# Optimization experiments

Hardware: AMD Instinct MI355X
Metric: run time of the kernel (lower is better)

## Reference

```python
import jax, jax.numpy as jnp
import numpy as np

B, T, NE, H = 4, 1024, 1024, 16
HS = NE // H  # 64
EPS = 0.00064


def setup_inputs() -> dict:
    key = jax.random.key(0)
    ks = jax.random.split(key, 30)
    def rn(k, shape, s):
        return jax.random.normal(k, shape, jnp.float32) * s
    d = {}
    d["x"] = jax.random.normal(ks[0], (B, T, NE), jnp.float32)
    d["time_maa_x"] = jax.random.uniform(ks[1], (NE,), jnp.float32)
    d["time_maa"] = jax.random.uniform(ks[2], (4, 1, 1, NE), jnp.float32)
    d["maa_w1"] = rn(ks[3], (128, NE), 0.02)   # 4 * D_MIX_LORA=32
    d["maa_w2"] = rn(ks[4], (4, 32, NE), 0.02)
    d["decay_w1"] = rn(ks[5], (64, NE), 0.02)
    d["decay_w2"] = rn(ks[6], (64, NE), 0.02)
    d["aaa_w1"] = rn(ks[7], (16, NE), 0.02)
    d["aaa_w2"] = rn(ks[8], (16, NE), 0.02)
    d["kkk_w1"] = rn(ks[9], (16, NE), 0.02)
    d["kkk_w2"] = rn(ks[10], (16, NE), 0.02)
    d["gate_w1"] = rn(ks[11], (128, NE), 0.02)
    d["gate_w2"] = rn(ks[12], (128, NE), 0.02)
    d["ma_w1"] = rn(ks[13], (16, NE), 0.02)
    d["ma_w2"] = rn(ks[14], (16, NE), 0.02)
    d["mk_w1"] = rn(ks[15], (16, NE), 0.02)
    d["mk_w2"] = rn(ks[16], (16, NE), 0.02)
    d["time_decay"] = jnp.linspace(-6.5, -1.5, NE, dtype=jnp.float32)  # decay_speed + 0.5 shape
    d["time_faaaa"] = rn(ks[17], (NE,), 0.02)
    d["time_aaaaa"] = rn(ks[18], (NE,), 0.02)
    d["time_misc_a"] = rn(ks[19], (NE,), 0.02)
    d["time_misc_k"] = rn(ks[20], (NE,), 0.02)
    d["Wr"] = rn(ks[21], (NE, NE), 0.5 / NE ** 0.5)
    d["Wk"] = rn(ks[22], (NE, NE), 0.05 / NE ** 0.5)
    d["Wv"] = rn(ks[23], (NE, NE), 0.5 / NE ** 0.5)
    d["Wo"] = rn(ks[24], (NE, NE), 1.0 / NE ** 0.5)
    d["ln_w"] = jnp.ones((NE,), jnp.float32)
    d["ln_b"] = jnp.zeros((NE,), jnp.float32)
    return d


def _forward(x, time_maa_x, time_maa, maa_w1, maa_w2, decay_w1, decay_w2,
             aaa_w1, aaa_w2, kkk_w1, kkk_w2, gate_w1, gate_w2,
             ma_w1, ma_w2, mk_w1, mk_w2, time_decay, time_faaaa, time_aaaaa,
             time_misc_a, time_misc_k, Wr, Wk, Wv, Wo, ln_w, ln_b):
    Bx, Tx, C = x.shape
    # token-shift delta: xx[t] = x[t-1] - x[t], with x[-1] = 0
    xx = jnp.pad(x, ((0, 0), (1, 0), (0, 0)))[:, :Tx] - x
    mix = x + xx * time_maa_x
    lo = jnp.tanh(jnp.einsum('btc,dc->btd', mix, maa_w1)).reshape(Bx, Tx, 4, 32)
    lo = jnp.einsum('btgk,gkc->gbtc', lo, maa_w2)           # [4,B,T,C]
    xm = x[None] + xx[None] * (lo + time_maa)               # time_maa broadcasts [4,1,1,C]
    xrg, xwa, xk, xv = xm[0], xm[1], xm[2], xm[3]

    r = xrg @ Wr.T
    g = jnp.tanh(xrg @ gate_w1.T) @ gate_w2
    k = xk @ Wk.T
    v = xv @ Wv.T
    w2 = jnp.tanh(xwa @ decay_w1.T) @ decay_w2
    w = -jax.nn.softplus(-(time_decay + w2)) - 0.5
    kk = k + jnp.tanh(xk @ kkk_w1.T) @ kkk_w2
    kkh = kk.reshape(Bx, Tx, H, HS)
    kk = (kkh / jnp.maximum(jnp.linalg.norm(kkh, axis=-1, keepdims=True), 1e-12)).reshape(Bx, Tx, C)
    a = jax.nn.sigmoid(time_aaaaa + (xwa @ aaa_w1.T) @ aaa_w2)
    ma = jax.nn.sigmoid(time_misc_a + (xwa @ ma_w1.T) @ ma_w2)
    k = k * ma + k * a * (1.0 - ma)
    mk = jax.nn.sigmoid(time_misc_k + (xk @ mk_w1.T) @ mk_w2)
    k = k * jnp.exp(w * mk)
    b = -kk * a

    # RWKV7 delta-rule recurrence: per-(B,H) HSxHS matrix state, scan over T
    def to_th(t):
        return t.reshape(Bx, Tx, H, HS).transpose(1, 0, 2, 3)  # [T,B,H,HS]
    qt, wt, kt, vt, at, bt = map(to_th, (r, w, k, v, kk, b))
    wt = jnp.exp(-jnp.exp(wt))

    def step(s, inp):
        q_, w_, k_, v_, a_, b_ = inp
        sa = jnp.einsum('bhij,bhj->bhi', s, a_)
        s = s * w_[:, :, None, :] + sa[..., None] * b_[:, :, None, :] + v_[..., None] * k_[:, :, None, :]
        return s, jnp.einsum('bhij,bhj->bhi', s, q_)

    s0 = jnp.zeros((Bx, H, HS, HS), x.dtype)
    _, y = jax.lax.scan(step, s0, (qt, wt, kt, vt, at, bt))
    y = y.transpose(1, 0, 2, 3).reshape(Bx, Tx, C)

    # GroupNorm with H groups, eps=0.00064
    yg = y.reshape(Bx, Tx, H, HS)
    mu = yg.mean(-1, keepdims=True)
    var = ((yg - mu) ** 2).mean(-1, keepdims=True)
    y = ((yg - mu) / jnp.sqrt(var + EPS)).reshape(Bx, Tx, C) * ln_w + ln_b

    # per-head bonus: (r.k * faaaa) v
    rk = (r.reshape(Bx, Tx, H, HS) * k.reshape(Bx, Tx, H, HS) * time_faaaa.reshape(H, HS)).sum(-1, keepdims=True)
    y = y + (rk * v.reshape(Bx, Tx, H, HS)).reshape(Bx, Tx, C)
    return (y * g) @ Wo.T


def reference(x, time_maa_x, time_maa, maa_w1, maa_w2, decay_w1, decay_w2,
              aaa_w1, aaa_w2, kkk_w1, kkk_w2, gate_w1, gate_w2,
              ma_w1, ma_w2, mk_w1, mk_w2, time_decay, time_faaaa, time_aaaaa,
              time_misc_a, time_misc_k, Wr, Wk, Wv, Wo, ln_w, ln_b):
    return _forward(x, time_maa_x, time_maa, maa_w1, maa_w2, decay_w1, decay_w2,
                    aaa_w1, aaa_w2, kkk_w1, kkk_w2, gate_w1, gate_w2,
                    ma_w1, ma_w2, mk_w1, mk_w2, time_decay, time_faaaa, time_aaaaa,
                    time_misc_a, time_misc_k, Wr, Wk, Wv, Wo, ln_w, ln_b)
```

## Files before the change

### kernel.cpp

```cpp
#include <hip/hip_runtime.h>
#include <cstdint>
#include <cstddef>

#define BB   4
#define TT   1024
#define CC   1024
#define HH   16
#define HSS  64
#define NNtok 4096
#define EPSGN 0.00064f
#define W2TS 192

typedef unsigned short bf16u;
typedef __attribute__((ext_vector_type(8))) short short8;
typedef __attribute__((ext_vector_type(4))) float f32x4;
#define SLOT 4194304ull

__device__ __forceinline__ float bf2f(bf16u u){
  union { unsigned int i; float f; } cv; cv.i = ((unsigned int)u) << 16; return cv.f;
}
__device__ __forceinline__ unsigned short f2bfbits(unsigned int x){
  return (unsigned short)((x + 0x7fffu + ((x >> 16) & 1u)) >> 16);
}
__device__ __forceinline__ bf16u f2bf(float f){
  union { float f; unsigned int i; } cv; cv.f = f;
  return f2bfbits(cv.i);
}
__device__ __forceinline__ void ld4bf(const bf16u* p, float* o){
  ushort4 u = *reinterpret_cast<const ushort4*>(p);
  o[0]=bf2f(u.x); o[1]=bf2f(u.y); o[2]=bf2f(u.z); o[3]=bf2f(u.w);
}
__device__ __forceinline__ void st4bf(bf16u* p, const float* v){
  ushort4 u; u.x=f2bf(v[0]); u.y=f2bf(v[1]); u.z=f2bf(v[2]); u.w=f2bf(v[3]);
  *reinterpret_cast<ushort4*>(p) = u;
}
__device__ __forceinline__ unsigned short f2h(float f){
  union { _Float16 h; unsigned short s; } c; c.h = (_Float16)f; return c.s;
}
__device__ __forceinline__ void st4h(bf16u* p, const float* v){
  ushort4 u; u.x=f2h(v[0]); u.y=f2h(v[1]); u.z=f2h(v[2]); u.w=f2h(v[3]);
  *reinterpret_cast<ushort4*>(p) = u;
}
__device__ __forceinline__ void ld4f(const float* p, float* o){
  float4 v = *reinterpret_cast<const float4*>(p);
  o[0]=v.x; o[1]=v.y; o[2]=v.z; o[3]=v.w;
}
__device__ __forceinline__ float sigm(float x){ return 1.f / (1.f + expf(-x)); }

__device__ __forceinline__ float bflo(unsigned int u){
  union { unsigned int i; float f; } c; c.i = u << 16; return c.f;
}
__device__ __forceinline__ float bfhi(unsigned int u){
  union { unsigned int i; float f; } c; c.i = u & 0xffff0000u; return c.f;
}
__device__ __forceinline__ float hlo(unsigned int u){
  union { unsigned short s; _Float16 h; } c; c.s = (unsigned short)(u & 0xffffu); return (float)c.h;
}
__device__ __forceinline__ float hhi(unsigned int u){
  union { unsigned short s; _Float16 h; } c; c.s = (unsigned short)(u >> 16); return (float)c.h;
}
__device__ __forceinline__ float hval(unsigned short s){
  union { unsigned short s; _Float16 h; } c; c.s = s; return (float)c.h;
}
__device__ __forceinline__ float dot4(const float* x, const float* y){
  return (x[0]*y[0] + x[1]*y[1]) + (x[2]*y[2] + x[3]*y[3]);
}

template<int CTRL>
__device__ __forceinline__ float dpp_add(float v){
  union { float f; int i; } a, b;
  a.f = v;
  b.i = __builtin_amdgcn_update_dpp(0, a.i, CTRL, 0xF, 0xF, true);
  return v + b.f;
}
__device__ __forceinline__ float red16(float v){
  v = dpp_add<0xB1>(v);
  v = dpp_add<0x4E>(v);
  v = dpp_add<0x124>(v);
  v = dpp_add<0x128>(v);
  return v;
}
__device__ __forceinline__ float red32(float v){
  v = red16(v);
  union { float f; int i; } x, y;
  x.f = v; y.f = v;
  asm volatile("" : "+v"(y.i));
  asm volatile("v_permlane16_swap_b32 %0, %1" : "+v"(x.i), "+v"(y.i));
  return x.f + y.f;
}

__global__ __launch_bounds__(256) void k_prep(const float* __restrict__ x,
                                              const float* __restrict__ tmx,
                                              bf16u* __restrict__ MIX){
  int e = (blockIdx.x * 256 + threadIdx.x) * 4;
  int n = e >> 10;
  int c = e & (CC - 1);
  int t = n & (TT - 1);
  float xf[4]; ld4f(x + e, xf);
  float pf[4] = {0.f, 0.f, 0.f, 0.f};
  if (t > 0) ld4f(x + e - CC, pf);
  float tm[4]; ld4f(tmx + c, tm);
  float mv[4];
  #pragma unroll
  for (int i = 0; i < 4; ++i) mv[i] = xf[i] + (pf[i] - xf[i]) * tm[i];
  st4bf(MIX + e, mv);
}

__global__ __launch_bounds__(256) void k_wconv1(
    const float* __restrict__ Wr, const float* __restrict__ Wk,
    const float* __restrict__ Wv,
    const float* __restrict__ maa_w1, const float* __restrict__ gate_w1,
    const float* __restrict__ decay_w1, const float* __restrict__ aaa_w1,
    const float* __restrict__ ma_w1, const float* __restrict__ kkk_w1,
    const float* __restrict__ mk_w1,
    const float* __restrict__ maa_w2, const float* __restrict__ decay_w2,
    bf16u* __restrict__ WrB, bf16u* __restrict__ WkB, bf16u* __restrict__ WvB,
    bf16u* __restrict__ W1B, bf16u* __restrict__ W2TB){
  int blk = blockIdx.x, tid = threadIdx.x;
  if (blk < 3072){
    const float* src = (blk < 1024) ? Wr : (blk < 2048) ? Wk : Wv;
    bf16u* dst = (blk < 1024) ? WrB : (blk < 2048) ? WkB : WvB;
    size_t e = (size_t)(blk & 1023) * 1024 + (size_t)tid * 4;
    float v[4]; ld4f(src + e, v);
    st4bf(dst + e, v);
  } else if (blk < 3456){
    int row = blk - 3072;
    const float* src;
    if      (row < 128) src = maa_w1   + (size_t)row * 1024;
    else if (row < 256) src = gate_w1  + (size_t)(row - 128) * 1024;
    else if (row < 320) src = decay_w1 + (size_t)(row - 256) * 1024;
    else if (row < 336) src = aaa_w1   + (size_t)(row - 320) * 1024;
    else if (row < 352) src = ma_w1    + (size_t)(row - 336) * 1024;
    else if (row < 368) src = kkk_w1   + (size_t)(row - 352) * 1024;
    else                src = mk_w1    + (size_t)(row - 368) * 1024;
    float v[4]; ld4f(src + tid * 4, v);
    st4bf(W1B + (size_t)row * 1024 + tid * 4, v);
  } else {
    int j = blk - 3456;
    const float* src = (j < 128) ? (maa_w2 + (size_t)j * 1024)
                                 : (decay_w2 + (size_t)(j - 128) * 1024);
    for (int c = tid; c < 1024; c += 256)
      W2TB[(size_t)c * W2TS + j] = f2bf(src[c]);
  }
}

__global__ __launch_bounds__(256) void k_wconv2(const float* __restrict__ Wo,
                                                const float* __restrict__ gate_w2,
                                                bf16u* __restrict__ WoB,
                                                bf16u* __restrict__ GW2T){
  int blk = blockIdx.x, tid = threadIdx.x;
  if (blk < 1024){
    size_t e = ((size_t)blk * 256 + tid) * 4;
    float v[4]; ld4f(Wo + e, v);
    st4bf(WoB + e, v);
  } else {
    int c = (blk - 1024) * 2 + (tid >> 7);
    int j = tid & 127;
    GW2T[(size_t)c * 128 + j] = f2bf(gate_w2[(size_t)j * CC + c]);
  }
}

template<bool OB>
__global__ __launch_bounds__(256) void k_gemm_mfma_b(const bf16u* __restrict__ X,
                                                     const bf16u* __restrict__ WB,
                                                     void* __restrict__ OUTv,
                                                     int Nd, int Kd, int act_n){
  __shared__ short As[2][128 * 40];
  __shared__ short Bs[2][128 * 40];
  const int tid  = threadIdx.x;
  const int lane = tid & 63;
  const int wv   = tid >> 6;
  const int wm   = wv >> 1, wn = wv & 1;
  const int bn0  = blockIdx.x * 128;
  const int bm0  = blockIdx.y * 128;
  const int l15  = lane & 15;
  const int quad = lane >> 4;

  f32x4 acc[4][4];
  #pragma unroll
  for (int mi = 0; mi < 4; ++mi)
    #pragma unroll
    for (int ni = 0; ni < 4; ++ni)
      #pragma unroll
      for (int rg = 0; rg < 4; ++rg) acc[mi][ni][rg] = 0.f;

  const int r    = tid >> 1;
  const int half = (tid & 1) * 16;

  const bf16u* wsrc = (bn0 + r < Nd) ? WB + (size_t)(bn0 + r) * Kd : nullptr;
  const bf16u* xsrc = X + (size_t)(bm0 + r) * Kd;

  uint4 xa = *(const uint4*)(xsrc + half);
  uint4 xb = *(const uint4*)(xsrc + half + 8);
  uint4 wa = make_uint4(0,0,0,0), wb = wa;
  if (wsrc){
    wa = *(const uint4*)(wsrc + half);
    wb = *(const uint4*)(wsrc + half + 8);
  }
  *(uint4*)&As[0][r * 40 + half]     = xa;
  *(uint4*)&As[0][r * 40 + half + 8] = xb;
  *(uint4*)&Bs[0][r * 40 + half]     = wa;
  *(uint4*)&Bs[0][r * 40 + half + 8] = wb;
  __syncthreads();

  const int NK = Kd >> 5;
  for (int k = 0; k < NK; ++k){
    const int cur = k & 1;
    if (k + 1 < NK){
      int k0 = (k + 1) << 5;
      xa = *(const uint4*)(xsrc + k0 + half);
      xb = *(const uint4*)(xsrc + k0 + half + 8);
      if (wsrc){
        wa = *(const uint4*)(wsrc + k0 + half);
        wb = *(const uint4*)(wsrc + k0 + half + 8);
      }
    }
    short8 af[4], bfg[4];
    #pragma unroll
    for (int mi = 0; mi < 4; ++mi)
      af[mi] = *(const short8*)&As[cur][(wm*64 + mi*16 + l15) * 40 + quad*8];
    #pragma unroll
    for (int ni = 0; ni < 4; ++ni)
      bfg[ni] = *(const short8*)&Bs[cur][(wn*64 + ni*16 + l15) * 40 + quad*8];
    #pragma unroll
    for (int mi = 0; mi < 4; ++mi)
      #pragma unroll
      for (int ni = 0; ni < 4; ++ni)
        acc[mi][ni] = __builtin_amdgcn_mfma_f32_16x16x32_bf16(af[mi], bfg[ni], acc[mi][ni], 0, 0, 0);
    if (k + 1 < NK){
      const int nxt = cur ^ 1;
      *(uint4*)&As[nxt][r * 40 + half]     = xa;
      *(uint4*)&As[nxt][r * 40 + half + 8] = xb;
      *(uint4*)&Bs[nxt][r * 40 + half]     = wa;
      *(uint4*)&Bs[nxt][r * 40 + half + 8] = wb;
      __syncthreads();
    }
  }

  #pragma unroll
  for (int mi = 0; mi < 4; ++mi){
    #pragma unroll
    for (int ni = 0; ni < 4; ++ni){
      int col = bn0 + wn*64 + ni*16 + l15;
      if (col >= Nd) continue;
      #pragma unroll
      for (int rg = 0; rg < 4; ++rg){
        int row = bm0 + wm*64 + mi*16 + quad*4 + rg;
        float v = acc[mi][ni][rg];
        if (col < act_n) v = tanhf(v);
        if (OB) ((bf16u*)OUTv)[(size_t)row * Nd + col] = f2bf(v);
        else    ((float*)OUTv)[(size_t)row * Nd + col] = v;
      }
    }
  }
}

template<int KD, int EP>
__global__ __launch_bounds__(256) void k_gemm_nn_b(const bf16u* __restrict__ A, int lda,
                                                   const bf16u* __restrict__ BT, int koff,
                                                   bf16u* __restrict__ OUT,
                                                   const float* __restrict__ x,
                                                   const float* __restrict__ tma_g){
  __shared__ short As[128 * (KD + 8)];
  __shared__ short Bs[128 * (KD + 8)];
  const int tid  = threadIdx.x;
  const int lane = tid & 63;
  const int wv   = tid >> 6;
  const int wm   = wv >> 1, wn = wv & 1;
  const int bn0  = blockIdx.x * 128;
  const int bm0  = blockIdx.y * 128;
  const int l15  = lane & 15;
  const int quad = lane >> 4;

  for (int idx = tid; idx < 128 * (KD / 8); idx += 256){
    int r  = idx / (KD / 8);
    int kc = (idx % (KD / 8)) * 8;
    *(uint4*)&As[r * (KD + 8) + kc] =
        *(const uint4*)(A + (size_t)(bm0 + r) * lda + kc);
  }
  for (int idx = tid; idx < 128 * (KD / 8); idx += 256){
    int cc_ = idx / (KD / 8);
    int kc  = (idx % (KD / 8)) * 8;
    *(uint4*)&Bs[cc_ * (KD + 8) + kc] =
        *(const uint4*)(BT + (size_t)(bn0 + cc_) * W2TS + koff + kc);
  }
  __syncthreads();

  f32x4 acc[4][4];
  #pragma unroll
  for (int mi = 0; mi < 4; ++mi)
    #pragma unroll
    for (int ni = 0; ni < 4; ++ni)
      #pragma unroll
      for (int rg = 0; rg < 4; ++rg) acc[mi][ni][rg] = 0.f;

  #pragma unroll
  for (int kk = 0; kk < KD; kk += 32){
    short8 af[4], bfg[4];
    #pragma unroll
    for (int mi = 0; mi < 4; ++mi)
      af[mi] = *(const short8*)&As[(wm*64 + mi*16 + l15) * (KD + 8) + kk + quad*8];
    #pragma unroll
    for (int ni = 0; ni < 4; ++ni)
      bfg[ni] = *(const short8*)&Bs[(wn*64 + ni*16 + l15) * (KD + 8) + kk + quad*8];
    #pragma unroll
    for (int mi = 0; mi < 4; ++mi)
      #pragma unroll
      for (int ni = 0; ni < 4; ++ni)
        acc[mi][ni] = __builtin_amdgcn_mfma_f32_16x16x32_bf16(af[mi], bfg[ni], acc[mi][ni], 0, 0, 0);
  }

  #pragma unroll
  for (int mi = 0; mi < 4; ++mi){
    #pragma unroll
    for (int ni = 0; ni < 4; ++ni){
      int col = bn0 + wn*64 + ni*16 + l15;
      float tm = (EP == 1) ? tma_g[col] : 0.f;
      #pragma unroll
      for (int rg = 0; rg < 4; ++rg){
        int row = bm0 + wm*64 + mi*16 + quad*4 + rg;
        float v = acc[mi][ni][rg];
        if (EP == 1){
          float xv = x[(size_t)row * CC + col];
          float xp = ((row & (TT - 1)) == 0) ? 0.f : x[(size_t)row * CC + col - CC];
          v = xv + (xp - xv) * (v + tm);
        }
        OUT[(size_t)row * CC + col] = f2bf(v);
      }
    }
  }
}

template<bool OB>
__global__ __launch_bounds__(256) void k_gemm_mfma(const bf16u* __restrict__ X,
                                                   const float* __restrict__ Wa,
                                                   const float* __restrict__ Wb,
                                                   const float* __restrict__ Wc,
                                                   int na, int nab,
                                                   void* __restrict__ OUTv,
                                                   int Nd, int Kd, int act_n){
  __shared__ short As[128 * 40];
  __shared__ short Bs[128 * 40];
  const int tid  = threadIdx.x;
  const int lane = tid & 63;
  const int wv   = tid >> 6;
  const int wm   = wv >> 1, wn = wv & 1;
  const int bn0  = blockIdx.x * 128;
  const int bm0  = blockIdx.y * 128;
  const int l15  = lane & 15;
  const int quad = lane >> 4;

  f32x4 acc[4][4];
  #pragma unroll
  for (int mi = 0; mi < 4; ++mi)
    #pragma unroll
    for (int ni = 0; ni < 4; ++ni)
      #pragma unroll
      for (int rg = 0; rg < 4; ++rg) acc[mi][ni][rg] = 0.f;

  const int r    = tid >> 1;
  const int half = (tid & 1) * 16;

  int rr = bn0 + r;
  const float* wsrc = nullptr;
  if (rr < na)        wsrc = Wa + (size_t)rr * Kd;
  else if (rr < nab)  wsrc = Wb + (size_t)(rr - na) * Kd;
  else if (rr < Nd)   wsrc = Wc + (size_t)(rr - nab) * Kd;
  const bf16u* xsrc = X + (size_t)(bm0 + r) * Kd;

  for (int k0 = 0; k0 < Kd; k0 += 32){
    uint4 xa = *(const uint4*)(xsrc + k0 + half);
    uint4 xb = *(const uint4*)(xsrc + k0 + half + 8);
    uint4 w0 = make_uint4(0,0,0,0), w1 = w0, w2 = w0, w3 = w0;
    if (wsrc){
      w0 = *(const uint4*)(wsrc + k0 + half);
      w1 = *(const uint4*)(wsrc + k0 + half + 4);
      w2 = *(const uint4*)(wsrc + k0 + half + 8);
      w3 = *(const uint4*)(wsrc + k0 + half + 12);
    }
    union { unsigned short s[8]; uint4 v; } p0, p1;
    p0.s[0]=f2bfbits(w0.x); p0.s[1]=f2bfbits(w0.y); p0.s[2]=f2bfbits(w0.z); p0.s[3]=f2bfbits(w0.w);
    p0.s[4]=f2bfbits(w1.x); p0.s[5]=f2bfbits(w1.y); p0.s[6]=f2bfbits(w1.z); p0.s[7]=f2bfbits(w1.w);
    p1.s[0]=f2bfbits(w2.x); p1.s[1]=f2bfbits(w2.y); p1.s[2]=f2bfbits(w2.z); p1.s[3]=f2bfbits(w2.w);
    p1.s[4]=f2bfbits(w3.x); p1.s[5]=f2bfbits(w3.y); p1.s[6]=f2bfbits(w3.z); p1.s[7]=f2bfbits(w3.w);

    *(uint4*)&As[r * 40 + half]     = xa;
    *(uint4*)&As[r * 40 + half + 8] = xb;
    *(uint4*)&Bs[r * 40 + half]     = p0.v;
    *(uint4*)&Bs[r * 40 + half + 8] = p1.v;
    __syncthreads();

    short8 af[4], bfg[4];
    #pragma unroll
    for (int mi = 0; mi < 4; ++mi)
      af[mi] = *(const short8*)&As[(wm*64 + mi*16 + l15) * 40 + quad*8];
    #pragma unroll
    for (int ni = 0; ni < 4; ++ni)
      bfg[ni] = *(const short8*)&Bs[(wn*64 + ni*16 + l15) * 40 + quad*8];
    #pragma unroll
    for (int mi = 0; mi < 4; ++mi)
      #pragma unroll
      for (int ni = 0; ni < 4; ++ni)
        acc[mi][ni] = __builtin_amdgcn_mfma_f32_16x16x32_bf16(af[mi], bfg[ni], acc[mi][ni], 0, 0, 0);
    __syncthreads();
  }

  #pragma unroll
  for (int mi = 0; mi < 4; ++mi){
    #pragma unroll
    for (int ni = 0; ni < 4; ++ni){
      int col = bn0 + wn*64 + ni*16 + l15;
      if (col >= Nd) continue;
      #pragma unroll
      for (int rg = 0; rg < 4; ++rg){
        int row = bm0 + wm*64 + mi*16 + quad*4 + rg;
        float v = acc[mi][ni][rg];
        if (col < act_n) v = tanhf(v);
        if (OB) ((bf16u*)OUTv)[(size_t)row * Nd + col] = f2bf(v);
        else    ((float*)OUTv)[(size_t)row * Nd + col] = v;
      }
    }
  }
}

template<int KD, int EP>
__global__ __launch_bounds__(256) void k_gemm_nn(const bf16u* __restrict__ A, int lda,
                                                 const float* __restrict__ B,
                                                 bf16u* __restrict__ OUT,
                                                 const float* __restrict__ x,
                                                 const float* __restrict__ tma_g){
  __shared__ short As[128 * (KD + 8)];
  __shared__ short Bs[128 * (KD + 8)];
  const int tid  = threadIdx.x;
  const int lane = tid & 63;
  const int wv   = tid >> 6;
  const int wm   = wv >> 1, wn = wv & 1;
  const int bn0  = blockIdx.x * 128;
  const int bm0  = blockIdx.y * 128;
  const int l15  = lane & 15;
  const int quad = lane >> 4;

  for (int idx = tid; idx < 128 * (KD / 8); idx += 256){
    int r  = idx / (KD / 8);
    int kc = (idx % (KD / 8)) * 8;
    *(uint4*)&As[r * (KD + 8) + kc] =
        *(const uint4*)(A + (size_t)(bm0 + r) * lda + kc);
  }
  for (int idx = tid; idx < KD * 128; idx += 256){
    int k = idx >> 7, c = idx & 127;
    Bs[c * (KD + 8) + k] = (short)f2bf(B[(size_t)k * CC + bn0 + c]);
  }
  __syncthreads();

  f32x4 acc[4][4];
  #pragma unroll
  for (int mi = 0; mi < 4; ++mi)
    #pragma unroll
    for (int ni = 0; ni < 4; ++ni)
      #pragma unroll
      for (int rg = 0; rg < 4; ++rg) acc[mi][ni][rg] = 0.f;

  #pragma unroll
  for (int kk = 0; kk < KD; kk += 32){
    short8 af[4], bfg[4];
    #pragma unroll
    for (int mi = 0; mi < 4; ++mi)
      af[mi] = *(const short8*)&As[(wm*64 + mi*16 + l15) * (KD + 8) + kk + quad*8];
    #pragma unroll
    for (int ni = 0; ni < 4; ++ni)
      bfg[ni] = *(const short8*)&Bs[(wn*64 + ni*16 + l15) * (KD + 8) + kk + quad*8];
    #pragma unroll
    for (int mi = 0; mi < 4; ++mi)
      #pragma unroll
      for (int ni = 0; ni < 4; ++ni)
        acc[mi][ni] = __builtin_amdgcn_mfma_f32_16x16x32_bf16(af[mi], bfg[ni], acc[mi][ni], 0, 0, 0);
  }

  #pragma unroll
  for (int mi = 0; mi < 4; ++mi){
    #pragma unroll
    for (int ni = 0; ni < 4; ++ni){
      int col = bn0 + wn*64 + ni*16 + l15;
      float tm = (EP == 1) ? tma_g[col] : 0.f;
      #pragma unroll
      for (int rg = 0; rg < 4; ++rg){
        int row = bm0 + wm*64 + mi*16 + quad*4 + rg;
        float v = acc[mi][ni][rg];
        if (EP == 1){
          float xv = x[(size_t)row * CC + col];
          float xp = ((row & (TT - 1)) == 0) ? 0.f : x[(size_t)row * CC + col - CC];
          v = xv + (xp - xv) * (v + tm);
        }
        OUT[(size_t)row * CC + col] = f2bf(v);
      }
    }
  }
}

template<int WMODE>
__global__ __launch_bounds__(256) void k_elem(bf16u* __restrict__ K0,
    const bf16u* __restrict__ P1, const bf16u* __restrict__ P2,
    const bf16u* __restrict__ W2A,
    const float* __restrict__ kw2, const float* __restrict__ aw2,
    const float* __restrict__ maw2, const float* __restrict__ mkw2,
    const float* __restrict__ td,  const float* __restrict__ taa,
    const float* __restrict__ tma, const float* __restrict__ tmk,
    const float* __restrict__ faaaa,
    bf16u* __restrict__ KKN, bf16u* __restrict__ Bb, bf16u* __restrict__ UX,
    float* __restrict__ WF,
    bf16u* __restrict__ Rq, float* __restrict__ Dsc, float* __restrict__ RKsc){
  int n0 = blockIdx.x * 4, tid = threadIdx.x;
  __shared__ float at_l[4][16], mat_l[4][16], kt_l[4][16], mkt_l[4][16];
  {
    int grp = tid >> 6, q = tid & 63, tt = q >> 4, j = q & 15;
    if (grp == 0)      at_l[tt][j]  = bf2f(P1[(size_t)(n0+tt)*96 + 64 + j]);
    else if (grp == 1) mat_l[tt][j] = bf2f(P1[(size_t)(n0+tt)*96 + 80 + j]);
    else if (grp == 2) kt_l[tt][j]  = bf2f(P2[(size_t)(n0+tt)*32 + j]);
    else               mkt_l[tt][j] = bf2f(P2[(size_t)(n0+tt)*32 + 16 + j]);
  }
  __syncthreads();
  int c  = tid * 4;
  int h  = tid >> 4;
  int lg = tid & 15;

  float kkk[4][4], aa[4][4], mam[4][4], mkm[4][4];
  #pragma unroll
  for (int tt = 0; tt < 4; ++tt)
    #pragma unroll
    for (int i = 0; i < 4; ++i){ kkk[tt][i]=0; aa[tt][i]=0; mam[tt][i]=0; mkm[tt][i]=0; }

  #pragma unroll 4
  for (int j = 0; j < 16; ++j){
    float wk[4], wa[4], wm[4], wq[4];
    ld4f(kw2  + (size_t)j*CC + c, wk);
    ld4f(aw2  + (size_t)j*CC + c, wa);
    ld4f(maw2 + (size_t)j*CC + c, wm);
    ld4f(mkw2 + (size_t)j*CC + c, wq);
    #pragma unroll
    for (int tt = 0; tt < 4; ++tt){
      float s1 = kt_l[tt][j], s2 = at_l[tt][j], s3 = mat_l[tt][j], s4 = mkt_l[tt][j];
      #pragma unroll
      for (int i = 0; i < 4; ++i){
        kkk[tt][i] += s1 * wk[i];
        aa[tt][i]  += s2 * wa[i];
        mam[tt][i] += s3 * wm[i];
        mkm[tt][i] += s4 * wq[i];
      }
    }
  }

  float td4[4], taa4[4], tma4[4], tmk4[4], fa4[4];
  ld4f(td + c, td4); ld4f(taa + c, taa4); ld4f(tma + c, tma4); ld4f(tmk + c, tmk4);
  ld4f(faaaa + c, fa4);

#define ELEM_TOKEN(TT_, E_, A_, B_, KF_, WD_) do{ \
    float k0a[4]; ld4bf(K0 + (E_), k0a); \
    float w2a[4]; ld4bf(W2A + (E_), w2a); \
    float ssq = 0.f; \
    _Pragma("unroll") \
    for (int i = 0; i < 4; ++i){ A_[i] = k0a[i] + kkk[TT_][i]; ssq += A_[i]*A_[i]; } \
    ssq = red16(ssq); \
    float rinv = 1.f / fmaxf(sqrtf(ssq), 1e-12f); \
    float outw_[4]; \
    _Pragma("unroll") \
    for (int i = 0; i < 4; ++i){ \
      float z  = td4[i] + w2a[i]; \
      float nz = -z; \
      float sp = (nz > 15.f) ? nz : log1pf(expf(nz)); \
      float w  = -sp - 0.5f; \
      float av  = sigm(taa4[i] + aa[TT_][i]); \
      float mav = sigm(tma4[i] + mam[TT_][i]); \
      float mkv = sigm(tmk4[i] + mkm[TT_][i]); \
      A_[i] *= rinv; \
      B_[i]  = -A_[i] * av; \
      KF_[i] = k0a[i] * (mav + av * (1.f - mav)) * expf(w * mkv); \
      float ou = -expf(w); \
      outw_[i] = ou; \
      if (WMODE == 1) WD_[i] = __expf(ou);               \
      else            WD_[i] = __expf(hval(f2h(ou)));    \
    } \
    st4bf(Bb + (E_), B_); \
    st4bf(K0 + (E_), KF_); \
    if (WMODE == 1) *(float4*)(WF + (E_)) = make_float4(WD_[0], WD_[1], WD_[2], WD_[3]); \
    else            st4h(UX + (E_), outw_); \
  }while(0)

  #pragma unroll
  for (int p = 0; p < 2; ++p){
    const int ttE = 2*p, ttO = ttE + 1;
    size_t eE = (size_t)(n0 + ttE) * CC + c;
    size_t eO = eE + CC;
    float aE[4], bE[4], kfE[4], wdE[4];
    float aO[4], bO[4], kfO[4], wdO[4];
    ELEM_TOKEN(ttE, eE, aE, bE, kfE, wdE);
    ELEM_TOKEN(ttO, eO, aO, bO, kfO, wdO);
    st4bf(KKN + eE, aE);

    float rE[4], rO[4];
    ld4bf(Rq + eE, rE); ld4bf(Rq + eO, rO);

    float rkE = red16(rE[0]*kfE[0]*fa4[0] + rE[1]*kfE[1]*fa4[1]
                    + rE[2]*kfE[2]*fa4[2] + rE[3]*kfE[3]*fa4[3]);
    float rkO = red16(rO[0]*kfO[0]*fa4[0] + rO[1]*kfO[1]*fa4[1]
                    + rO[2]*kfO[2]*fa4[2] + rO[3]*kfO[3]*fa4[3]);

    float c1 = red16(dot4(bE, aO));
    float d  = red16(dot4(kfE, aO));
    float u1[4];
    #pragma unroll
    for (int i = 0; i < 4; ++i) u1[i] = wdE[i]*aO[i] + c1*aE[i];
    st4bf(KKN + eO, u1);

    float cq = red16(dot4(bE, rE));
    float e1 = red16(dot4(kfE, rE));
    float qe[4];
    #pragma unroll
    for (int i = 0; i < 4; ++i) qe[i] = wdE[i]*rE[i] + cq*aE[i];
    st4bf(Rq + eE, qe);

    float cz  = red16(dot4(bO, rO));
    float e21 = red16(dot4(kfO, rO));
    float z[4];
    #pragma unroll
    for (int i = 0; i < 4; ++i) z[i] = wdO[i]*rO[i] + cz*aO[i];
    float cy  = red16(dot4(bE, z));
    float e20 = red16(dot4(kfE, z));
    float qo[4];
    #pragma unroll
    for (int i = 0; i < 4; ++i) qo[i] = wdE[i]*z[i] + cy*aE[i];
    st4bf(Rq + eO, qo);

    if (lg == 0){
      size_t pr = (size_t)((n0 + ttE) >> 1);
      float4 dv; dv.x = d; dv.y = e1; dv.z = e20; dv.w = e21;
      *(float4*)(Dsc + (pr * HH + h) * 4) = dv;
      RKsc[(size_t)(n0 + ttE) * HH + h] = rkE;
      RKsc[(size_t)(n0 + ttO) * HH + h] = rkO;
    }
  }
#undef ELEM_TOKEN
}

template<int WMODE>
__global__ __launch_bounds__(256) void k_rec(const bf16u* __restrict__ Qp,
                                             const bf16u* __restrict__ WT,
                                             const float* __restrict__ WF,
                                             const bf16u* __restrict__ KFt,
                                             const bf16u* __restrict__ Vt,
                                             const bf16u* __restrict__ Aa,
                                             const bf16u* __restrict__ Bv,
                                             const float* __restrict__ Dsc,
                                             bf16u* __restrict__ Y){
  const int p   = blockIdx.x;
  const int g   = (p & 7) | ((p >> 6) << 3);
  const int oct = (p >> 3) & 7;
  const int b   = g >> 4;
  const int h   = g & 15;
  const int tid = threadIdx.x;
  const int l31 = tid & 31;
  const int i   = oct * 8 + (tid >> 5);
  const size_t base0 = (size_t)(b * TT) * CC + h * HSS;
  const size_t colb  = base0 + l31 * 2;
  const size_t rowb  = base0 + i;
  const size_t dscb  = ((size_t)(b * (TT/2)) * HH + h) * 4;

  float S0 = 0.f, S1 = 0.f;

  unsigned int qEA,qOA,aEA,uOA,kEA,kOA,bEA,bOA,wEA,wOA; float2 fEA,fOA; unsigned short vEA,vOA; float4 dA;
  unsigned int qEB,qOB,aEB,uOB,kEB,kOB,bEB,bOB,wEB,wOB; float2 fEB,fOB; unsigned short vEB,vOB; float4 dB;
  unsigned int qEC,qOC,aEC,uOC,kEC,kOC,bEC,bOC,wEC,wOC; float2 fEC,fOC; unsigned short vEC,vOC; float4 dC;
  unsigned int qED,qOD,aED,uOD,kED,kOD,bED,bOD,wED,wOD; float2 fED,fOD; unsigned short vED,vOD; float4 dD;

#define PL(S, T_) do{ \
    size_t cE_ = colb + (size_t)(T_) * CC, cO_ = cE_ + CC; \
    qE##S = *(const unsigned int*)(Qp  + cE_); qO##S = *(const unsigned int*)(Qp  + cO_); \
    aE##S = *(const unsigned int*)(Aa  + cE_); uO##S = *(const unsigned int*)(Aa  + cO_); \
    kE##S = *(const unsigned int*)(KFt + cE_); kO##S = *(const unsigned int*)(KFt + cO_); \
    bE##S = *(const unsigned int*)(Bv  + cE_); bO##S = *(const unsigned int*)(Bv  + cO_); \
    if (WMODE == 1){ \
      fE##S = *(const float2*)(WF + cE_); fO##S = *(const float2*)(WF + cO_); \
    } else { \
      wE##S = *(const unsigned int*)(WT + cE_); wO##S = *(const unsigned int*)(WT + cO_); \
    } \
    vE##S = Vt[rowb + (size_t)(T_) * CC]; \
    vO##S = Vt[rowb + (size_t)(T_ + 1) * CC]; \
    d##S  = *(const float4*)(Dsc + dscb + (size_t)((T_) >> 1) * (HH*4)); \
  }while(0)

#define PSTEP(S, T_) do{ \
    float a0=bflo(aE##S), a1=bfhi(aE##S); \
    float u0=bflo(uO##S), u1=bfhi(uO##S); \
    float g0=bflo(qE##S), g1=bfhi(qE##S); \
    float o0=bflo(qO##S), o1=bfhi(qO##S); \
    float pE_ = fmaf(S1, a1, S0 * a0); \
    float pO_ = fmaf(S1, u1, S0 * u0); \
    float yE_ = fmaf(S1, g1, S0 * g0); \
    float yO_ = fmaf(S1, o1, S0 * o0); \
    pE_ = red32(pE_); \
    pO_ = red32(pO_); \
    yE_ = red32(yE_); \
    yO_ = red32(yO_); \
    float vEf = bf2f(vE##S), vOf = bf2f(vO##S); \
    float saE = pE_; \
    float saO = fmaf(d##S.x, vEf, pO_); \
    float ypE = fmaf(d##S.y, vEf, yE_); \
    float ypO = fmaf(d##S.z, vEf, fmaf(d##S.w, vOf, yO_)); \
    float k0=bflo(kE##S), k1=bfhi(kE##S); \
    float b0=bflo(bE##S), b1=bfhi(bE##S); \
    float w0, w1; \
    if (WMODE == 1){ w0=fE##S.x; w1=fE##S.y; } \
    else { w0=__expf(hlo(wE##S)); w1=__expf(hhi(wE##S)); } \
    S0 = fmaf(S0, w0, fmaf(saE, b0, vEf * k0)); \
    S1 = fmaf(S1, w1, fmaf(saE, b1, vEf * k1)); \
    float ko0=bflo(kO##S), ko1=bfhi(kO##S); \
    float bo0=bflo(bO##S), bo1=bfhi(bO##S); \
    float wo0, wo1; \
    if (WMODE == 1){ wo0=fO##S.x; wo1=fO##S.y; } \
    else { wo0=__expf(hlo(wO##S)); wo1=__expf(hhi(wO##S)); } \
    S0 = fmaf(S0, wo0, fmaf(saO, bo0, vOf * ko0)); \
    S1 = fmaf(S1, wo1, fmaf(saO, bo1, vOf * ko1)); \
    if (l31 == 0){ \
      Y[rowb + (size_t)(T_) * CC]     = f2bf(ypE); \
      Y[rowb + (size_t)(T_ + 1) * CC] = f2bf(ypO); \
    } \
  }while(0)

  PL(A, 0); PL(B, 2); PL(C, 4); PL(D, 6);
  for (int t = 0; t < TT; t += 8){
    PSTEP(A, t);
    if (t + 8  < TT) PL(A, t + 8);
    PSTEP(B, t + 2);
    if (t + 10 < TT) PL(B, t + 10);
    PSTEP(C, t + 4);
    if (t + 12 < TT) PL(C, t + 12);
    PSTEP(D, t + 6);
    if (t + 14 < TT) PL(D, t + 14);
  }
#undef PL
#undef PSTEP
}

__global__ __launch_bounds__(256) void k_post(const bf16u* __restrict__ Y,
                                              const bf16u* __restrict__ Vt,
                                              const bf16u* __restrict__ GV,
                                              const float* __restrict__ lnw,
                                              const float* __restrict__ lnb,
                                              const float* __restrict__ RKsc,
                                              bf16u* __restrict__ YG){
  int n = blockIdx.x, tid = threadIdx.x;
  int c = tid * 4;
  size_t e = (size_t)n * CC + c;

  float ya[4]; ld4bf(Y + e, ya);
  float s = ya[0] + ya[1] + ya[2] + ya[3];
  s = red16(s);
  float mu = s * (1.f / 64.f);
  float d[4], vs = 0.f;
  #pragma unroll
  for (int i = 0; i < 4; ++i){ d[i] = ya[i] - mu; vs += d[i] * d[i]; }
  vs = red16(vs);
  float rstd = rsqrtf(vs * (1.f / 64.f) + EPSGN);

  float rk = RKsc[(size_t)n * HH + (tid >> 4)];

  float va[4]; ld4bf(Vt + e, va);
  float lw4[4], lb4[4];
  ld4f(lnw + c, lw4); ld4f(lnb + c, lb4);
  float g[4]; ld4bf(GV + e, g);
  float o[4];
  #pragma unroll
  for (int i = 0; i < 4; ++i){
    float yn = d[i] * rstd * lw4[i] + lb4[i] + rk * va[i];
    o[i] = yn * g[i];
  }
  st4bf(YG + e, o);
}

extern "C" void kernel_launch(void* const* d_in, const int* in_sizes, int n_in,
                              void* d_out, int out_size, void* d_ws, size_t ws_size,
                              hipStream_t stream){
  (void)in_sizes; (void)n_in; (void)out_size;
  const float* x        = (const float*)d_in[0];
  const float* tmx      = (const float*)d_in[1];
  const float* tmaa     = (const float*)d_in[2];
  const float* maa_w1   = (const float*)d_in[3];
  const float* maa_w2   = (const float*)d_in[4];
  const float* decay_w1 = (const float*)d_in[5];
  const float* decay_w2 = (const float*)d_in[6];
  const float* aaa_w1   = (const float*)d_in[7];
  const float* aaa_w2   = (const float*)d_in[8];
  const float* kkk_w1   = (const float*)d_in[9];
  const float* kkk_w2   = (const float*)d_in[10];
  const float* gate_w1  = (const float*)d_in[11];
  const float* gate_w2  = (const float*)d_in[12];
  const float* ma_w1    = (const float*)d_in[13];
  const float* ma_w2    = (const float*)d_in[14];
  const float* mk_w1    = (const float*)d_in[15];
  const float* mk_w2    = (const float*)d_in[16];
  const float* t_decay  = (const float*)d_in[17];
  const float* t_faaaa  = (const float*)d_in[18];
  const float* t_aaaaa  = (const float*)d_in[19];
  const float* t_misc_a = (const float*)d_in[20];
  const float* t_misc_k = (const float*)d_in[21];
  const float* Wr       = (const float*)d_in[22];
  const float* Wk       = (const float*)d_in[23];
  const float* Wv       = (const float*)d_in[24];
  const float* Wo       = (const float*)d_in[25];
  const float* ln_w     = (const float*)d_in[26];
  const float* ln_b     = (const float*)d_in[27];

  bf16u* bw  = (bf16u*)d_ws;
  bf16u* MIX = bw + 0*SLOT;
  bf16u* X0  = bw + 0*SLOT;
  bf16u* KKN = bw + 0*SLOT;
  bf16u* YG  = bw + 0*SLOT;
  bf16u* X1  = bw + 1*SLOT;
  bf16u* Bb  = bw + 1*SLOT;
  bf16u* GV  = bw + 1*SLOT;
  bf16u* X2  = bw + 2*SLOT;
  bf16u* UX  = bw + 2*SLOT;
  bf16u* X3  = bw + 3*SLOT;
  bf16u* W2A = bw + 3*SLOT;
  bf16u* Yb  = bw + 3*SLOT;
  bf16u* R   = bw + 4*SLOT;
  bf16u* K0  = bw + 5*SLOT;
  bf16u* V   = bw + 6*SLOT;
  char*  wsb = (char*)d_ws;
  bf16u* LO  = (bf16u*)(wsb + (56ull<<20));
  bf16u* GT  = (bf16u*)(wsb + (57ull<<20));
  bf16u* P1  = (bf16u*)(wsb + (58ull<<20));
  bf16u* P2  = (bf16u*)(wsb + (58ull<<20) + (768ull<<10));
  float* Dsc = (float*)(wsb + (59ull<<20));
  float* RKsc= (float*)(wsb + (59ull<<20) + (512ull<<10));
  float* WF  = (float*)(wsb + (60ull<<20));
  bf16u* WrB = (bf16u*)(wsb + (60ull<<20));
  bf16u* WkB = (bf16u*)(wsb + (62ull<<20));
  bf16u* WvB = (bf16u*)(wsb + (64ull<<20));
  bf16u* W1B = (bf16u*)(wsb + (66ull<<20));
  bf16u* W2TB= (bf16u*)(wsb + (67ull<<20));
  bf16u* WoB = (bf16u*)(wsb + (60ull<<20));
  bf16u* GW2T= (bf16u*)(wsb + (62ull<<20));
  const bool fast = ws_size >= (77ull<<20);

  if (fast){
    k_wconv1<<<3648, 256, 0, stream>>>(Wr, Wk, Wv, maa_w1, gate_w1, decay_w1,
                                       aaa_w1, ma_w1, kkk_w1, mk_w1,
                                       maa_w2, decay_w2,
                                       WrB, WkB, WvB, W1B, W2TB);
    k_prep<<<4096, 256, 0, stream>>>(x, tmx, MIX);
    k_gemm_mfma_b<true><<<dim3(1,32),256,0,stream>>>(MIX, W1B, LO, 128, CC, 128);
    bf16u* XMs[4] = {X0, X1, X2, X3};
    for (int g = 0; g < 4; ++g)
      k_gemm_nn_b<32,1><<<dim3(8,32),256,0,stream>>>(LO + g*32, 128, W2TB, g*32,
                                                     XMs[g], x, tmaa + (size_t)g*CC);
    k_gemm_mfma_b<true><<<dim3(8,32),256,0,stream>>>(X0, WrB, R,  CC, CC, 0);
    k_gemm_mfma_b<true><<<dim3(8,32),256,0,stream>>>(X2, WkB, K0, CC, CC, 0);
    k_gemm_mfma_b<true><<<dim3(8,32),256,0,stream>>>(X3, WvB, V,  CC, CC, 0);
    k_gemm_mfma_b<true><<<dim3(1,32),256,0,stream>>>(X0, W1B + 128*1024, GT, 128, CC, 128);
    k_gemm_mfma_b<true><<<dim3(1,32),256,0,stream>>>(X1, W1B + 256*1024, P1, 96,  CC, 64);
    k_gemm_mfma_b<true><<<dim3(1,32),256,0,stream>>>(X2, W1B + 352*1024, P2, 32,  CC, 16);
    k_gemm_nn_b<64,0><<<dim3(8,32),256,0,stream>>>(P1, 96, W2TB, 128, W2A, nullptr, nullptr);
    k_elem<1><<<1024, 256, 0, stream>>>(K0, P1, P2, W2A,
                                        kkk_w2, aaa_w2, ma_w2, mk_w2,
                                        t_decay, t_aaaaa, t_misc_a, t_misc_k, t_faaaa,
                                        KKN, Bb, UX, WF, R, Dsc, RKsc);
    k_rec<1><<<512, 256, 0, stream>>>(R, UX, WF, K0, V, KKN, Bb, Dsc, Yb);
    k_wconv2<<<1536, 256, 0, stream>>>(Wo, gate_w2, WoB, GW2T);
    k_gemm_mfma_b<true><<<dim3(8,32),256,0,stream>>>(GT, GW2T, GV, CC, 128, 0);
    k_post<<<4096, 256, 0, stream>>>(Yb, V, GV, ln_w, ln_b, RKsc, YG);
    k_gemm_mfma_b<false><<<dim3(8,32),256,0,stream>>>(YG, WoB, d_out, CC, CC, 0);
  } else {
    k_prep<<<4096, 256, 0, stream>>>(x, tmx, MIX);
    k_gemm_mfma<true><<<dim3(1,32),256,0,stream>>>(MIX, maa_w1, maa_w1, maa_w1,
                                                   128, 128, LO, 128, CC, 128);
    bf16u* XMs[4] = {X0, X1, X2, X3};
    for (int g = 0; g < 4; ++g)
      k_gemm_nn<32,1><<<dim3(8,32),256,0,stream>>>(LO + g*32, 128,
                                                   maa_w2 + (size_t)g*32*CC,
                                                   XMs[g], x, tmaa + (size_t)g*CC);
    k_gemm_mfma<true><<<dim3(8,32),256,0,stream>>>(X0, Wr, Wr, Wr, CC, CC, R,  CC, CC, 0);
    k_gemm_mfma<true><<<dim3(8,32),256,0,stream>>>(X2, Wk, Wk, Wk, CC, CC, K0, CC, CC, 0);
    k_gemm_mfma<true><<<dim3(8,32),256,0,stream>>>(X3, Wv, Wv, Wv, CC, CC, V,  CC, CC, 0);
    k_gemm_mfma<true><<<dim3(1,32),256,0,stream>>>(X0, gate_w1, gate_w1, gate_w1,
                                                   128, 128, GT, 128, CC, 128);
    k_gemm_mfma<true><<<dim3(1,32),256,0,stream>>>(X1, decay_w1, aaa_w1, ma_w1,
                                                   64, 80, P1, 96, CC, 64);
    k_gemm_mfma<true><<<dim3(1,32),256,0,stream>>>(X2, kkk_w1, mk_w1, mk_w1,
                                                   16, 32, P2, 32, CC, 16);
    k_gemm_nn<64,0><<<dim3(8,32),256,0,stream>>>(P1, 96, decay_w2, W2A, nullptr, nullptr);
    k_elem<0><<<1024, 256, 0, stream>>>(K0, P1, P2, W2A,
                                        kkk_w2, aaa_w2, ma_w2, mk_w2,
                                        t_decay, t_aaaaa, t_misc_a, t_misc_k, t_faaaa,
                                        KKN, Bb, UX, WF, R, Dsc, RKsc);
    k_rec<0><<<512, 256, 0, stream>>>(R, UX, WF, K0, V, KKN, Bb, Dsc, Yb);
    k_gemm_nn<128,0><<<dim3(8,32),256,0,stream>>>(GT, 128, gate_w2, GV, nullptr, nullptr);
    k_post<<<4096, 256, 0, stream>>>(Yb, V, GV, ln_w, ln_b, RKsc, YG);
    k_gemm_mfma<false><<<dim3(8,32),256,0,stream>>>(YG, Wo, Wo, Wo, CC, CC, d_out, CC, CC, 0);
  }
}
```

Before: 677.2 us.

## Halve GEMM M-tile to 64 rows and batch small GEMM launches via grid z

Replaces the 128x128 bf16 MFMA GEMM tile with a 64x128 tile, doubling the number of blocks for every projection GEMM so the 256 CUs get more work. The four maa mixing GEMMs are merged into one launch over blockIdx.z, and the three LoRA down-projections likewise. This targets under-occupancy and launch overhead on small grids, at the cost of less operand reuse per block (more reloads of the weight tile). The X0..X3 buffers are assumed to sit SLOT apart.

```diff
diff --git a/kernel.cpp b/kernel.cpp
--- a/kernel.cpp
+++ b/kernel.cpp
@@ -160,47 +160,45 @@
   }
 }
 
+#define B64_ASZ (64*40)
+#define B64_BSZ (128*40)
 template<bool OB>
-__global__ __launch_bounds__(256) void k_gemm_mfma_b(const bf16u* __restrict__ X,
-                                                     const bf16u* __restrict__ WB,
-                                                     void* __restrict__ OUTv,
-                                                     int Nd, int Kd, int act_n){
-  __shared__ short As[2][128 * 40];
-  __shared__ short Bs[2][128 * 40];
+__device__ __forceinline__ void gemm_b64_body(const bf16u* __restrict__ X,
+                                              const bf16u* __restrict__ WB,
+                                              void* __restrict__ OUTv,
+                                              int Nd, int Kd, int act_n,
+                                              short* __restrict__ As,
+                                              short* __restrict__ Bs,
+                                              int bn0, int bm0){
   const int tid  = threadIdx.x;
   const int lane = tid & 63;
   const int wv   = tid >> 6;
   const int wm   = wv >> 1, wn = wv & 1;
-  const int bn0  = blockIdx.x * 128;
-  const int bm0  = blockIdx.y * 128;
   const int l15  = lane & 15;
   const int quad = lane >> 4;
 
-  f32x4 acc[4][4];
-  #pragma unroll
-  for (int mi = 0; mi < 4; ++mi)
+  f32x4 acc[2][4];
+  #pragma unroll
+  for (int mi = 0; mi < 2; ++mi)
     #pragma unroll
     for (int ni = 0; ni < 4; ++ni)
       #pragma unroll
       for (int rg = 0; rg < 4; ++rg) acc[mi][ni][rg] = 0.f;
 
-  const int r    = tid >> 1;
-  const int half = (tid & 1) * 16;
-
-  const bf16u* wsrc = (bn0 + r < Nd) ? WB + (size_t)(bn0 + r) * Kd : nullptr;
-  const bf16u* xsrc = X + (size_t)(bm0 + r) * Kd;
-
-  uint4 xa = *(const uint4*)(xsrc + half);
-  uint4 xb = *(const uint4*)(xsrc + half + 8);
+  const int ra = tid >> 2, ka = (tid & 3) * 8;
+  const int rb = tid >> 1, kb = (tid & 1) * 16;
+  const bf16u* xsrc = X + (size_t)(bm0 + ra) * Kd;
+  const bf16u* wsrc = (bn0 + rb < Nd) ? WB + (size_t)(bn0 + rb) * Kd : nullptr;
+
+  uint4 xa = *(const uint4*)(xsrc + ka);
   uint4 wa = make_uint4(0,0,0,0), wb = wa;
   if (wsrc){
-    wa = *(const uint4*)(wsrc + half);
-    wb = *(const uint4*)(wsrc + half + 8);
-  }
-  *(uint4*)&As[0][r * 40 + half]     = xa;
-  *(uint4*)&As[0][r * 40 + half + 8] = xb;
-  *(uint4*)&Bs[0][r * 40 + half]     = wa;
-  *(uint4*)&Bs[0][r * 40 + half + 8] = wb;
+    wa = *(const uint4*)(wsrc + kb);
+    wb = *(const uint4*)(wsrc + kb + 8);
+  }
+  *(uint4*)&As[ra * 40 + ka]      = xa;
+  *(uint4*)&Bs[rb * 40 + kb]      = wa;
+  *(uint4*)&Bs[rb * 40 + kb + 8]  = wb;
   __syncthreads();
 
   const int NK = Kd >> 5;
@@ -208,44 +206,42 @@
     const int cur = k & 1;
     if (k + 1 < NK){
       int k0 = (k + 1) << 5;
-      xa = *(const uint4*)(xsrc + k0 + half);
-      xb = *(const uint4*)(xsrc + k0 + half + 8);
+      xa = *(const uint4*)(xsrc + k0 + ka);
       if (wsrc){
-        wa = *(const uint4*)(wsrc + k0 + half);
-        wb = *(const uint4*)(wsrc + k0 + half + 8);
+        wa = *(const uint4*)(wsrc + k0 + kb);
+        wb = *(const uint4*)(wsrc + k0 + kb + 8);
       }
     }
-    short8 af[4], bfg[4];
-    #pragma unroll
-    for (int mi = 0; mi < 4; ++mi)
-      af[mi] = *(const short8*)&As[cur][(wm*64 + mi*16 + l15) * 40 + quad*8];
+    short8 af[2], bfg[4];
+    #pragma unroll
+    for (int mi = 0; mi < 2; ++mi)
+      af[mi] = *(const short8*)&As[cur*B64_ASZ + (wm*32 + mi*16 + l15) * 40 + quad*8];
     #pragma unroll
     for (int ni = 0; ni < 4; ++ni)
-      bfg[ni] = *(const short8*)&Bs[cur][(wn*64 + ni*16 + l15) * 40 + quad*8];
-    #pragma unroll
-    for (int mi = 0; mi < 4; ++mi)
+      bfg[ni] = *(const short8*)&Bs[cur*B64_BSZ + (wn*64 + ni*16 + l15) * 40 + quad*8];
+    #pragma unroll
+    for (int mi = 0; mi < 2; ++mi)
       #pragma unroll
       for (int ni = 0; ni < 4; ++ni)
         acc[mi][ni] = __builtin_amdgcn_mfma_f32_16x16x32_bf16(af[mi], bfg[ni], acc[mi][ni], 0, 0, 0);
     if (k + 1 < NK){
       const int nxt = cur ^ 1;
-      *(uint4*)&As[nxt][r * 40 + half]     = xa;
-      *(uint4*)&As[nxt][r * 40 + half + 8] = xb;
-      *(uint4*)&Bs[nxt][r * 40 + half]     = wa;
-      *(uint4*)&Bs[nxt][r * 40 + half + 8] = wb;
+      *(uint4*)&As[nxt*B64_ASZ + ra * 40 + ka]     = xa;
+      *(uint4*)&Bs[nxt*B64_BSZ + rb * 40 + kb]     = wa;
+      *(uint4*)&Bs[nxt*B64_BSZ + rb * 40 + kb + 8] = wb;
       __syncthreads();
     }
   }
 
   #pragma unroll
-  for (int mi = 0; mi < 4; ++mi){
+  for (int mi = 0; mi < 2; ++mi){
     #pragma unroll
     for (int ni = 0; ni < 4; ++ni){
       int col = bn0 + wn*64 + ni*16 + l15;
       if (col >= Nd) continue;
       #pragma unroll
       for (int rg = 0; rg < 4; ++rg){
-        int row = bm0 + wm*64 + mi*16 + quad*4 + rg;
+        int row = bm0 + wm*32 + mi*16 + quad*4 + rg;
         float v = acc[mi][ni][rg];
         if (col < act_n) v = tanhf(v);
         if (OB) ((bf16u*)OUTv)[(size_t)row * Nd + col] = f2bf(v);
@@ -255,20 +251,49 @@
   }
 }
 
+template<bool OB>
+__global__ __launch_bounds__(256) void k_gemm_b64(const bf16u* __restrict__ X,
+                                                  const bf16u* __restrict__ WB,
+                                                  void* __restrict__ OUTv,
+                                                  int Nd, int Kd, int act_n){
+  __shared__ short As[2*B64_ASZ];
+  __shared__ short Bs[2*B64_BSZ];
+  gemm_b64_body<OB>(X, WB, OUTv, Nd, Kd, act_n, As, Bs,
+                    blockIdx.x * 128, blockIdx.y * 64);
+}
+
+__global__ __launch_bounds__(256) void k_gemm_b64_lora(const bf16u* __restrict__ X0,
+                                                       const bf16u* __restrict__ X1,
+                                                       const bf16u* __restrict__ X2,
+                                                       const bf16u* __restrict__ W1B,
+                                                       bf16u* __restrict__ GT,
+                                                       bf16u* __restrict__ P1,
+                                                       bf16u* __restrict__ P2){
+  __shared__ short As[2*B64_ASZ];
+  __shared__ short Bs[2*B64_BSZ];
+  const int z = blockIdx.z;
+  const int bm0 = blockIdx.y * 64;
+  if (z == 0)
+    gemm_b64_body<true>(X0, W1B + 128*1024, GT, 128, CC, 128, As, Bs, 0, bm0);
+  else if (z == 1)
+    gemm_b64_body<true>(X1, W1B + 256*1024, P1, 96, CC, 64, As, Bs, 0, bm0);
+  else
+    gemm_b64_body<true>(X2, W1B + 352*1024, P2, 32, CC, 16, As, Bs, 0, bm0);
+}
+
 template<int KD, int EP>
-__global__ __launch_bounds__(256) void k_gemm_nn_b(const bf16u* __restrict__ A, int lda,
-                                                   const bf16u* __restrict__ BT, int koff,
-                                                   bf16u* __restrict__ OUT,
-                                                   const float* __restrict__ x,
-                                                   const float* __restrict__ tma_g){
-  __shared__ short As[128 * (KD + 8)];
-  __shared__ short Bs[128 * (KD + 8)];
+__device__ __forceinline__ void gemm_nn_body(const bf16u* __restrict__ A, int lda,
+                                             const bf16u* __restrict__ BT, int koff,
+                                             bf16u* __restrict__ OUT,
+                                             const float* __restrict__ x,
+                                             const float* __restrict__ tma_g,
+                                             short* __restrict__ As,
+                                             short* __restrict__ Bs,
+                                             int bn0, int bm0){
   const int tid  = threadIdx.x;
   const int lane = tid & 63;
   const int wv   = tid >> 6;
   const int wm   = wv >> 1, wn = wv & 1;
-  const int bn0  = blockIdx.x * 128;
-  const int bm0  = blockIdx.y * 128;
   const int l15  = lane & 15;
   const int quad = lane >> 4;
 
@@ -329,6 +354,31 @@
       }
     }
   }
+}
+
+template<int KD, int EP>
+__global__ __launch_bounds__(256) void k_gemm_nn_b(const bf16u* __restrict__ A, int lda,
+                                                   const bf16u* __restrict__ BT, int koff,
+                                                   bf16u* __restrict__ OUT,
+                                                   const float* __restrict__ x,
+                                                   const float* __restrict__ tma_g){
+  __shared__ short As[128 * (KD + 8)];
+  __shared__ short Bs[128 * (KD + 8)];
+  gemm_nn_body<KD, EP>(A, lda, BT, koff, OUT, x, tma_g, As, Bs,
+                       blockIdx.x * 128, blockIdx.y * 128);
+}
+
+__global__ __launch_bounds__(256) void k_gemm_nn_b4(const bf16u* __restrict__ LO,
+                                                    const bf16u* __restrict__ BT,
+                                                    bf16u* __restrict__ X0base,
+                                                    const float* __restrict__ x,
+                                                    const float* __restrict__ tmaa){
+  __shared__ short As[128 * 40];
+  __shared__ short Bs[128 * 40];
+  const int z = blockIdx.z;
+  gemm_nn_body<32, 1>(LO + z*32, 128, BT, z*32, X0base + (size_t)z*SLOT,
+                      x, tmaa + (size_t)z*CC, As, Bs,
+                      blockIdx.x * 128, blockIdx.y * 128);
 }
 
 template<bool OB>
@@ -848,17 +898,12 @@
                                        maa_w2, decay_w2,
                                        WrB, WkB, WvB, W1B, W2TB);
     k_prep<<<4096, 256, 0, stream>>>(x, tmx, MIX);
-    k_gemm_mfma_b<true><<<dim3(1,32),256,0,stream>>>(MIX, W1B, LO, 128, CC, 128);
-    bf16u* XMs[4] = {X0, X1, X2, X3};
-    for (int g = 0; g < 4; ++g)
-      k_gemm_nn_b<32,1><<<dim3(8,32),256,0,stream>>>(LO + g*32, 128, W2TB, g*32,
-                                                     XMs[g], x, tmaa + (size_t)g*CC);
-    k_gemm_mfma_b<true><<<dim3(8,32),256,0,stream>>>(X0, WrB, R,  CC, CC, 0);
-    k_gemm_mfma_b<true><<<dim3(8,32),256,0,stream>>>(X2, WkB, K0, CC, CC, 0);
-    k_gemm_mfma_b<true><<<dim3(8,32),256,0,stream>>>(X3, WvB, V,  CC, CC, 0);
-    k_gemm_mfma_b<true><<<dim3(1,32),256,0,stream>>>(X0, W1B + 128*1024, GT, 128, CC, 128);
-    k_gemm_mfma_b<true><<<dim3(1,32),256,0,stream>>>(X1, W1B + 256*1024, P1, 96,  CC, 64);
-    k_gemm_mfma_b<true><<<dim3(1,32),256,0,stream>>>(X2, W1B + 352*1024, P2, 32,  CC, 16);
+    k_gemm_b64<true><<<dim3(1,64),256,0,stream>>>(MIX, W1B, LO, 128, CC, 128);
+    k_gemm_nn_b4<<<dim3(8,32,4),256,0,stream>>>(LO, W2TB, X0, x, tmaa);
+    k_gemm_b64<true><<<dim3(8,64),256,0,stream>>>(X0, WrB, R,  CC, CC, 0);
+    k_gemm_b64<true><<<dim3(8,64),256,0,stream>>>(X2, WkB, K0, CC, CC, 0);
+    k_gemm_b64<true><<<dim3(8,64),256,0,stream>>>(X3, WvB, V,  CC, CC, 0);
+    k_gemm_b64_lora<<<dim3(1,64,3),256,0,stream>>>(X0, X1, X2, W1B, GT, P1, P2);
     k_gemm_nn_b<64,0><<<dim3(8,32),256,0,stream>>>(P1, 96, W2TB, 128, W2A, nullptr, nullptr);
     k_elem<1><<<1024, 256, 0, stream>>>(K0, P1, P2, W2A,
                                         kkk_w2, aaa_w2, ma_w2, mk_w2,
@@ -866,9 +911,9 @@
                                         KKN, Bb, UX, WF, R, Dsc, RKsc);
     k_rec<1><<<512, 256, 0, stream>>>(R, UX, WF, K0, V, KKN, Bb, Dsc, Yb);
     k_wconv2<<<1536, 256, 0, stream>>>(Wo, gate_w2, WoB, GW2T);
-    k_gemm_mfma_b<true><<<dim3(8,32),256,0,stream>>>(GT, GW2T, GV, CC, 128, 0);
+    k_gemm_b64<true><<<dim3(8,64),256,0,stream>>>(GT, GW2T, GV, CC, 128, 0);
     k_post<<<4096, 256, 0, stream>>>(Yb, V, GV, ln_w, ln_b, RKsc, YG);
-    k_gemm_mfma_b<false><<<dim3(8,32),256,0,stream>>>(YG, WoB, d_out, CC, CC, 0);
+    k_gemm_b64<false><<<dim3(8,64),256,0,stream>>>(YG, WoB, d_out, CC, CC, 0);
   } else {
     k_prep<<<4096, 256, 0, stream>>>(x, tmx, MIX);
     k_gemm_mfma<true><<<dim3(1,32),256,0,stream>>>(MIX, maa_w1, maa_w1, maa_w1,
```

Result: faster. 589.0 us (-13.0%).
